# Optimization experiments

Measured on AMD Instinct MI355X. Metric: run time of the kernel, lower is better.

Reference implementation:

```python
import jax, jax.numpy as jnp
import numpy as np

B, T, IN, H, OUT = 64, 256, 512, 1024, 512

def setup_inputs() -> dict:
    key = jax.random.key(0)
    k1, k2, k3, k4 = jax.random.split(key, 4)
    xs = jax.random.normal(k1, (B, T, IN), dtype=jnp.float32)
    # fused gate projections (order: i, f, g, o), scaled like lecun_normal-ish init
    Wi = jax.random.normal(k2, (IN, 4 * H), dtype=jnp.float32) * (1.0 / np.sqrt(IN))
    Wh = jax.random.normal(k3, (H, 4 * H), dtype=jnp.float32) * (1.0 / np.sqrt(H))
    b = jnp.zeros((4 * H,), dtype=jnp.float32)
    Wo = jax.random.normal(k4, (H, OUT), dtype=jnp.float32) * (1.0 / np.sqrt(H))
    bo = jnp.zeros((OUT,), dtype=jnp.float32)
    return {"xs": xs, "Wi": Wi, "Wh": Wh, "b": b, "Wo": Wo, "bo": bo}

def _lstm_scan(xs, Wi, Wh, b):
    # Precompute the input projection for all timesteps at once: [B, T, 4H]
    xp = jnp.einsum('bti,ih->bth', xs, Wi)
    xp = jnp.transpose(xp, (1, 0, 2))  # [T, B, 4H] for scan over time
    h0 = jnp.zeros((xs.shape[0], Wh.shape[0]), dtype=xs.dtype)
    c0 = jnp.zeros_like(h0)
    Hdim = Wh.shape[0]

    def step(carry, xp_t):
        c, h = carry
        gates = xp_t + h @ Wh + b  # [B, 4H]
        i, f, g, o = jnp.split(gates, 4, axis=-1)  # flax order: i, f, g, o
        c_new = jax.nn.sigmoid(f) * c + jax.nn.sigmoid(i) * jnp.tanh(g)
        h_new = jax.nn.sigmoid(o) * jnp.tanh(c_new)
        return (c_new, h_new), h_new

    (_, _), hs = jax.lax.scan(step, (c0, h0), xp)
    return jnp.transpose(hs, (1, 0, 2))  # [B, T, H]

def reference(xs, Wi, Wh, b, Wo, bo):
    zs = _lstm_scan(xs, Wi, Wh, b)          # [B, T, H]
    logits = jnp.einsum('bth,ho->bto', zs, Wo) + bo  # [B, T, OUT]
    return logits
```

## Files before the change

kernel.cpp:

```cpp
#include <hip/hip_runtime.h>
#include <hip/hip_cooperative_groups.h>


#define B_   64
#define T_   256
#define IN_  512
#define H_   1024
#define G4_  4096
#define OUT_ 512
#define KTOT 1536

typedef __bf16 bf8v  __attribute__((ext_vector_type(8)));
typedef float  f4v   __attribute__((ext_vector_type(4)));

__device__ __forceinline__ float sigm(float x) { return 1.f / (1.f + __expf(-x)); }
__device__ __forceinline__ float tanh_f(float x) { return 1.f - 2.f / (__expf(2.f * x) + 1.f); }

__device__ __forceinline__ void store_bf16_wt(__bf16* p, __bf16 v) {
    union { __bf16 b; unsigned short s; } cv; cv.b = v;
    unsigned w = cv.s;
    asm volatile("global_store_short %0, %1, off sc0 sc1"
                 :: "v"(p), "v"(w) : "memory");
}

#define X_PRE(tt, xa0, xa1)                                                   \
    {                                                                         \
        const float* xrow = xs + ((size_t)rowA * T_ + (size_t)(tt)) * IN_ + kq; \
        _Pragma("unroll")                                                     \
        for (int ks = 0; ks < 16; ++ks) {                                     \
            f4v v0 = *(const f4v*)(xrow + ks * 32);                           \
            f4v v1 = *(const f4v*)(xrow + ks * 32 + 4);                       \
            bf8v ah, al;                                                      \
            _Pragma("unroll")                                                 \
            for (int j = 0; j < 4; ++j) {                                     \
                __bf16 h0 = (__bf16)v0[j], h1 = (__bf16)v1[j];                \
                ah[j] = h0;  ah[4 + j] = h1;                                  \
                al[j]     = (__bf16)(v0[j] - (float)h0);                      \
                al[4 + j] = (__bf16)(v1[j] - (float)h1);                      \
            }                                                                 \
            bf8v w = *(const bf8v*)&Wlds[c][ks * 32 + kq];                    \
            xa0 = __builtin_amdgcn_mfma_f32_16x16x32_bf16(ah, w, xa0, 0, 0, 0); \
            xa1 = __builtin_amdgcn_mfma_f32_16x16x32_bf16(al, w, xa1, 0, 0, 0); \
        }                                                                     \
    }

__global__ void __launch_bounds__(256, 1)
lstm_fused(const float* __restrict__ xs, const float* __restrict__ Wi,
           const float* __restrict__ Wh, const float* __restrict__ bias,
           const float* __restrict__ Wo, const float* __restrict__ bo,
           float* __restrict__ out, __bf16* __restrict__ hws,
           unsigned* __restrict__ flags)
{
    __shared__ __bf16 Wlds[16][KTOT + 8];
    __shared__ float  gbuf[64][17];
    __shared__ float  obuf[4][16][17];

    const int tid = threadIdx.x;
    const int blk = blockIdx.x;
    const int j0  = blk * 4;
    const int ob0 = (blk >> 5) * 8;
    const int oc0 = (blk & 31) * 16;

    for (int idx = tid; idx < 16 * KTOT; idx += 256) {
        int k = idx >> 4, c = idx & 15;
        int gc = (c >> 2) * H_ + j0 + (c & 3);
        float w = (k < IN_) ? Wi[(size_t)k * G4_ + gc]
                            : Wh[(size_t)(k - IN_) * G4_ + gc];
        Wlds[c][k] = (__bf16)w;
    }
    __syncthreads();

    const int lane = tid & 63;
    const int wave = tid >> 6;
    const int c    = lane & 15;
    const int quad = lane >> 4;
    const int rowA = wave * 16 + c;
    const int kq   = quad * 8;

    const float biasv = bias[(c >> 2) * H_ + j0 + (c & 3)];

    bf8v wof[8];
    #pragma unroll
    for (int kk = 0; kk < 8; ++kk) {
        int kbase = wave * 256 + kk * 32 + kq;
        #pragma unroll
        for (int j = 0; j < 8; ++j)
            wof[kk][j] = (__bf16)Wo[(size_t)(kbase + j) * OUT_ + oc0 + c];
    }

    float c_reg = 0.f;
    const int bb = tid >> 2;
    const int jo = tid & 3;

    f4v xacc0 = {0.f, 0.f, 0.f, 0.f};
    f4v xacc1 = {0.f, 0.f, 0.f, 0.f};
    X_PRE(0, xacc0, xacc1);

    const size_t bufsz = (size_t)2 * B_ * H_;

    for (int t = 0; t < T_; ++t) {
        const int br = (t + 2) % 3;
        const int bw = t % 3;
        const __bf16* hhi_p = hws + (size_t)br * bufsz;
        const __bf16* hlo_p = hhi_p + B_ * H_;
        __bf16* hhi_c = hws + (size_t)bw * bufsz;
        __bf16* hlo_c = hhi_c + B_ * H_;

        f4v acc0 = xacc0;
        f4v acc1 = xacc1;
        if (t > 0) {
            const __bf16* hh = hhi_p + (size_t)rowA * H_ + kq;
            const __bf16* hl = hlo_p + (size_t)rowA * H_ + kq;
            #pragma unroll
            for (int ks = 0; ks < 32; ++ks) {
                bf8v ah = *(const bf8v*)(hh + ks * 32);
                bf8v al = *(const bf8v*)(hl + ks * 32);
                bf8v w  = *(const bf8v*)&Wlds[c][IN_ + ks * 32 + kq];
                acc0 = __builtin_amdgcn_mfma_f32_16x16x32_bf16(ah, w, acc0, 0, 0, 0);
                acc1 = __builtin_amdgcn_mfma_f32_16x16x32_bf16(al, w, acc1, 0, 0, 0);
            }
        }
        f4v acc = acc0 + acc1;
        #pragma unroll
        for (int r = 0; r < 4; ++r)
            gbuf[wave * 16 + quad * 4 + r][c] = acc[r] + biasv;
        __syncthreads();

        {
            float gi = gbuf[bb][jo];
            float gf = gbuf[bb][4 + jo];
            float gg = gbuf[bb][8 + jo];
            float go = gbuf[bb][12 + jo];
            c_reg = sigm(gf) * c_reg + sigm(gi) * tanh_f(gg);
            float hn = sigm(go) * tanh_f(c_reg);
            __bf16 hh = (__bf16)hn;
            store_bf16_wt(&hhi_c[(size_t)bb * H_ + j0 + jo], hh);
            store_bf16_wt(&hlo_c[(size_t)bb * H_ + j0 + jo], (__bf16)(hn - (float)hh));
        }

        __syncthreads();
        const unsigned tgt = (unsigned)(t + 1);
        if (tid == 0) {
            unsigned* p = &flags[blk * 16];
            asm volatile("global_store_dword %0, %1, off sc0 sc1"
                         :: "v"(p), "v"(tgt) : "memory");
        }

        if (t > 0) {
            f4v oac = {0.f, 0.f, 0.f, 0.f};
            #pragma unroll
            for (int kk = 0; kk < 8; ++kk) {
                int kbase = wave * 256 + kk * 32 + kq;
                bf8v ah = {}, al = {};
                if (c < 8) {
                    ah = *(const bf8v*)&hhi_p[(size_t)(ob0 + c) * H_ + kbase];
                    al = *(const bf8v*)&hlo_p[(size_t)(ob0 + c) * H_ + kbase];
                }
                oac = __builtin_amdgcn_mfma_f32_16x16x32_bf16(ah, wof[kk], oac, 0, 0, 0);
                oac = __builtin_amdgcn_mfma_f32_16x16x32_bf16(al, wof[kk], oac, 0, 0, 0);
            }
            #pragma unroll
            for (int r = 0; r < 4; ++r)
                obuf[wave][quad * 4 + r][c] = oac[r];
        }
        __syncthreads();

        if (t > 0 && tid < 128) {
            int m = tid >> 4, cc = tid & 15;
            float v = obuf[0][m][cc] + obuf[1][m][cc] + obuf[2][m][cc] + obuf[3][m][cc]
                    + bo[oc0 + cc];
            out[(((size_t)(ob0 + m)) * T_ + (t - 1)) * OUT_ + oc0 + cc] = v;
        }

        xacc0 = (f4v){0.f, 0.f, 0.f, 0.f};
        xacc1 = (f4v){0.f, 0.f, 0.f, 0.f};
        if (t + 1 < T_) {
            X_PRE(t + 1, xacc0, xacc1);
        }
        asm volatile("" ::: "memory");

        if (tid < 64) {
            const int lane2 = tid;
            for (;;) {
                unsigned m0 = __hip_atomic_load(&flags[(lane2 * 4 + 0) * 16],
                                                __ATOMIC_RELAXED, __HIP_MEMORY_SCOPE_AGENT);
                unsigned m1 = __hip_atomic_load(&flags[(lane2 * 4 + 1) * 16],
                                                __ATOMIC_RELAXED, __HIP_MEMORY_SCOPE_AGENT);
                unsigned m2 = __hip_atomic_load(&flags[(lane2 * 4 + 2) * 16],
                                                __ATOMIC_RELAXED, __HIP_MEMORY_SCOPE_AGENT);
                unsigned m3 = __hip_atomic_load(&flags[(lane2 * 4 + 3) * 16],
                                                __ATOMIC_RELAXED, __HIP_MEMORY_SCOPE_AGENT);
                bool ok = (m0 >= tgt) & (m1 >= tgt) & (m2 >= tgt) & (m3 >= tgt);
                if (__all(ok)) break;
                __builtin_amdgcn_s_sleep(1);
            }
            __builtin_amdgcn_fence(__ATOMIC_ACQUIRE, "agent");
        }
        __syncthreads();
    }

    {
        const __bf16* hhi_l = hws;
        const __bf16* hlo_l = hws + B_ * H_;
        f4v oac = {0.f, 0.f, 0.f, 0.f};
        #pragma unroll
        for (int kk = 0; kk < 8; ++kk) {
            int kbase = wave * 256 + kk * 32 + kq;
            bf8v ah = {}, al = {};
            if (c < 8) {
                ah = *(const bf8v*)&hhi_l[(size_t)(ob0 + c) * H_ + kbase];
                al = *(const bf8v*)&hlo_l[(size_t)(ob0 + c) * H_ + kbase];
            }
            oac = __builtin_amdgcn_mfma_f32_16x16x32_bf16(ah, wof[kk], oac, 0, 0, 0);
            oac = __builtin_amdgcn_mfma_f32_16x16x32_bf16(al, wof[kk], oac, 0, 0, 0);
        }
        #pragma unroll
        for (int r = 0; r < 4; ++r)
            obuf[wave][quad * 4 + r][c] = oac[r];
        __syncthreads();
        if (tid < 128) {
            int m = tid >> 4, cc = tid & 15;
            float v = obuf[0][m][cc] + obuf[1][m][cc] + obuf[2][m][cc] + obuf[3][m][cc]
                    + bo[oc0 + cc];
            out[(((size_t)(ob0 + m)) * T_ + (T_ - 1)) * OUT_ + oc0 + cc] = v;
        }
    }
}

extern "C" void kernel_launch(void* const* d_in, const int* in_sizes, int n_in,
                              void* d_out, int out_size, void* d_ws, size_t ws_size,
                              hipStream_t stream) {
    const float* xs = (const float*)d_in[0];
    const float* Wi = (const float*)d_in[1];
    const float* Wh = (const float*)d_in[2];
    const float* b  = (const float*)d_in[3];
    const float* Wo = (const float*)d_in[4];
    const float* bo = (const float*)d_in[5];
    float* out = (float*)d_out;

    unsigned* flags = (unsigned*)d_ws;
    __bf16*   hws   = (__bf16*)((char*)d_ws + 65536);

    hipMemsetAsync(d_ws, 0, 32768, stream);

    void* args[] = {(void*)&xs, (void*)&Wi, (void*)&Wh, (void*)&b,
                    (void*)&Wo, (void*)&bo, (void*)&out, (void*)&hws,
                    (void*)&flags};
    hipLaunchCooperativeKernel((void*)lstm_fused, dim3(256), dim3(256), args, 0, stream);
}
```

Before: 4.142 ms.

## Switch LSTM recurrence to single fp16 MFMA with pipelined hidden-state loads

```diff
diff --git a/kernel.cpp b/kernel.cpp
--- a/kernel.cpp
+++ b/kernel.cpp
@@ -10,50 +10,70 @@
 #define OUT_ 512
 #define KTOT 1536
 
-typedef __bf16 bf8v  __attribute__((ext_vector_type(8)));
-typedef float  f4v   __attribute__((ext_vector_type(4)));
+typedef _Float16 f16x8 __attribute__((ext_vector_type(8)));
+typedef float    f4v   __attribute__((ext_vector_type(4)));
 
 __device__ __forceinline__ float sigm(float x) { return 1.f / (1.f + __expf(-x)); }
 __device__ __forceinline__ float tanh_f(float x) { return 1.f - 2.f / (__expf(2.f * x) + 1.f); }
 
-__device__ __forceinline__ void store_bf16_wt(__bf16* p, __bf16 v) {
-    union { __bf16 b; unsigned short s; } cv; cv.b = v;
-    unsigned w = cv.s;
+#define GLOAD(dst, p) \
+    asm volatile("global_load_dwordx4 %0, %1, off sc0 sc1" \
+                 : "=v"(dst) : "v"(p))
+
+#define VM_WAIT(n) do { \
+    asm volatile("s_waitcnt vmcnt(" #n ")"); \
+    __builtin_amdgcn_sched_barrier(0); \
+} while (0)
+
+__device__ __forceinline__ void store_f16_wt(_Float16* p, _Float16 v) {
+    unsigned short s = __builtin_bit_cast(unsigned short, v);
+    unsigned w = s;
     asm volatile("global_store_short %0, %1, off sc0 sc1"
                  :: "v"(p), "v"(w) : "memory");
 }
 
-#define X_PRE(tt, xa0, xa1)                                                   \
+#define X_PRE(tt, xa)                                                         \
     {                                                                         \
         const float* xrow = xs + ((size_t)rowA * T_ + (size_t)(tt)) * IN_ + kq; \
         _Pragma("unroll")                                                     \
         for (int ks = 0; ks < 16; ++ks) {                                     \
             f4v v0 = *(const f4v*)(xrow + ks * 32);                           \
             f4v v1 = *(const f4v*)(xrow + ks * 32 + 4);                       \
-            bf8v ah, al;                                                      \
+            f16x8 a;                                                          \
             _Pragma("unroll")                                                 \
             for (int j = 0; j < 4; ++j) {                                     \
-                __bf16 h0 = (__bf16)v0[j], h1 = (__bf16)v1[j];                \
-                ah[j] = h0;  ah[4 + j] = h1;                                  \
-                al[j]     = (__bf16)(v0[j] - (float)h0);                      \
-                al[4 + j] = (__bf16)(v1[j] - (float)h1);                      \
+                a[j]     = (_Float16)v0[j];                                   \
+                a[4 + j] = (_Float16)v1[j];                                   \
             }                                                                 \
-            bf8v w = *(const bf8v*)&Wlds[c][ks * 32 + kq];                    \
-            xa0 = __builtin_amdgcn_mfma_f32_16x16x32_bf16(ah, w, xa0, 0, 0, 0); \
-            xa1 = __builtin_amdgcn_mfma_f32_16x16x32_bf16(al, w, xa1, 0, 0, 0); \
+            f16x8 w = *(const f16x8*)&Wlds[c][ks * 32 + kq];                  \
+            xa = __builtin_amdgcn_mfma_f32_16x16x32_f16(a, w, xa, 0, 0, 0);   \
         }                                                                     \
+    }
+
+#define GISSUE(Areg, kb)                                                      \
+    _Pragma("unroll")                                                         \
+    for (int i = 0; i < 8; ++i) {                                             \
+        GLOAD(Areg[i], hp + ((kb) + i) * 32);                                 \
+    }
+
+#define GCONSUME(Areg, kb)                                                    \
+    _Pragma("unroll")                                                         \
+    for (int i = 0; i < 8; ++i) {                                             \
+        f16x8 w = *(const f16x8*)&Wlds[c][IN_ + ((kb) + i) * 32 + kq];        \
+        acc = __builtin_amdgcn_mfma_f32_16x16x32_f16(                         \
+            __builtin_bit_cast(f16x8, Areg[i]), w, acc, 0, 0, 0);             \
     }
 
 __global__ void __launch_bounds__(256, 1)
 lstm_fused(const float* __restrict__ xs, const float* __restrict__ Wi,
            const float* __restrict__ Wh, const float* __restrict__ bias,
            const float* __restrict__ Wo, const float* __restrict__ bo,
-           float* __restrict__ out, __bf16* __restrict__ hws,
+           float* __restrict__ out, _Float16* __restrict__ hws,
            unsigned* __restrict__ flags)
 {
-    __shared__ __bf16 Wlds[16][KTOT + 8];
-    __shared__ float  gbuf[64][17];
-    __shared__ float  obuf[4][16][17];
+    __shared__ _Float16 Wlds[16][KTOT + 8];
+    __shared__ float    gbuf[64][17];
+    __shared__ float    obuf[4][16][17];
 
     const int tid = threadIdx.x;
     const int blk = blockIdx.x;
@@ -66,7 +86,7 @@
         int gc = (c >> 2) * H_ + j0 + (c & 3);
         float w = (k < IN_) ? Wi[(size_t)k * G4_ + gc]
                             : Wh[(size_t)(k - IN_) * G4_ + gc];
-        Wlds[c][k] = (__bf16)w;
+        Wlds[c][k] = (_Float16)w;
     }
     __syncthreads();
 
@@ -79,48 +99,48 @@
 
     const float biasv = bias[(c >> 2) * H_ + j0 + (c & 3)];
 
-    bf8v wof[8];
+    f16x8 wof[8];
     #pragma unroll
     for (int kk = 0; kk < 8; ++kk) {
         int kbase = wave * 256 + kk * 32 + kq;
         #pragma unroll
         for (int j = 0; j < 8; ++j)
-            wof[kk][j] = (__bf16)Wo[(size_t)(kbase + j) * OUT_ + oc0 + c];
+            wof[kk][j] = (_Float16)Wo[(size_t)(kbase + j) * OUT_ + oc0 + c];
     }
 
     float c_reg = 0.f;
     const int bb = tid >> 2;
     const int jo = tid & 3;
 
-    f4v xacc0 = {0.f, 0.f, 0.f, 0.f};
-    f4v xacc1 = {0.f, 0.f, 0.f, 0.f};
-    X_PRE(0, xacc0, xacc1);
-
-    const size_t bufsz = (size_t)2 * B_ * H_;
+    f4v xacc = {0.f, 0.f, 0.f, 0.f};
+    X_PRE(0, xacc);
+
+    const size_t bufsz = (size_t)B_ * H_;
 
     for (int t = 0; t < T_; ++t) {
+        asm volatile("" ::: "memory");
         const int br = (t + 2) % 3;
         const int bw = t % 3;
-        const __bf16* hhi_p = hws + (size_t)br * bufsz;
-        const __bf16* hlo_p = hhi_p + B_ * H_;
-        __bf16* hhi_c = hws + (size_t)bw * bufsz;
-        __bf16* hlo_c = hhi_c + B_ * H_;
-
-        f4v acc0 = xacc0;
-        f4v acc1 = xacc1;
+        const _Float16* h_p = hws + (size_t)br * bufsz;
+        _Float16*       h_c = hws + (size_t)bw * bufsz;
+
+        f4v acc = xacc;
         if (t > 0) {
-            const __bf16* hh = hhi_p + (size_t)rowA * H_ + kq;
-            const __bf16* hl = hlo_p + (size_t)rowA * H_ + kq;
-            #pragma unroll
-            for (int ks = 0; ks < 32; ++ks) {
-                bf8v ah = *(const bf8v*)(hh + ks * 32);
-                bf8v al = *(const bf8v*)(hl + ks * 32);
-                bf8v w  = *(const bf8v*)&Wlds[c][IN_ + ks * 32 + kq];
-                acc0 = __builtin_amdgcn_mfma_f32_16x16x32_bf16(ah, w, acc0, 0, 0, 0);
-                acc1 = __builtin_amdgcn_mfma_f32_16x16x32_bf16(al, w, acc1, 0, 0, 0);
-            }
-        }
-        f4v acc = acc0 + acc1;
+            const _Float16* hp = h_p + (size_t)rowA * H_ + kq;
+            f4v A0[8], A1[8];
+            GISSUE(A0, 0);
+            GISSUE(A1, 8);
+            VM_WAIT(8);
+            GCONSUME(A0, 0);
+            GISSUE(A0, 16);
+            VM_WAIT(8);
+            GCONSUME(A1, 8);
+            GISSUE(A1, 24);
+            VM_WAIT(8);
+            GCONSUME(A0, 16);
+            VM_WAIT(0);
+            GCONSUME(A1, 24);
+        }
         #pragma unroll
         for (int r = 0; r < 4; ++r)
             gbuf[wave * 16 + quad * 4 + r][c] = acc[r] + biasv;
@@ -133,9 +153,7 @@
             float go = gbuf[bb][12 + jo];
             c_reg = sigm(gf) * c_reg + sigm(gi) * tanh_f(gg);
             float hn = sigm(go) * tanh_f(c_reg);
-            __bf16 hh = (__bf16)hn;
-            store_bf16_wt(&hhi_c[(size_t)bb * H_ + j0 + jo], hh);
-            store_bf16_wt(&hlo_c[(size_t)bb * H_ + j0 + jo], (__bf16)(hn - (float)hh));
+            store_f16_wt(&h_c[(size_t)bb * H_ + j0 + jo], (_Float16)hn);
         }
 
         __syncthreads();
@@ -147,18 +165,22 @@
         }
 
         if (t > 0) {
+            f4v Oh[8];
+            #pragma unroll
+            for (int kk = 0; kk < 8; ++kk)
+                Oh[kk] = (f4v){0.f, 0.f, 0.f, 0.f};
+            const _Float16* orow = h_p + (size_t)(ob0 + c) * H_;
+            if (c < 8) {
+                #pragma unroll
+                for (int kk = 0; kk < 8; ++kk)
+                    GLOAD(Oh[kk], orow + wave * 256 + kk * 32 + kq);
+            }
+            VM_WAIT(0);
             f4v oac = {0.f, 0.f, 0.f, 0.f};
             #pragma unroll
-            for (int kk = 0; kk < 8; ++kk) {
-                int kbase = wave * 256 + kk * 32 + kq;
-                bf8v ah = {}, al = {};
-                if (c < 8) {
-                    ah = *(const bf8v*)&hhi_p[(size_t)(ob0 + c) * H_ + kbase];
-                    al = *(const bf8v*)&hlo_p[(size_t)(ob0 + c) * H_ + kbase];
-                }
-                oac = __builtin_amdgcn_mfma_f32_16x16x32_bf16(ah, wof[kk], oac, 0, 0, 0);
-                oac = __builtin_amdgcn_mfma_f32_16x16x32_bf16(al, wof[kk], oac, 0, 0, 0);
-            }
+            for (int kk = 0; kk < 8; ++kk)
+                oac = __builtin_amdgcn_mfma_f32_16x16x32_f16(
+                    __builtin_bit_cast(f16x8, Oh[kk]), wof[kk], oac, 0, 0, 0);
             #pragma unroll
             for (int r = 0; r < 4; ++r)
                 obuf[wave][quad * 4 + r][c] = oac[r];
@@ -172,10 +194,9 @@
             out[(((size_t)(ob0 + m)) * T_ + (t - 1)) * OUT_ + oc0 + cc] = v;
         }
 
-        xacc0 = (f4v){0.f, 0.f, 0.f, 0.f};
-        xacc1 = (f4v){0.f, 0.f, 0.f, 0.f};
+        xacc = (f4v){0.f, 0.f, 0.f, 0.f};
         if (t + 1 < T_) {
-            X_PRE(t + 1, xacc0, xacc1);
+            X_PRE(t + 1, xacc);
         }
         asm volatile("" ::: "memory");
 
@@ -194,26 +215,28 @@
                 if (__all(ok)) break;
                 __builtin_amdgcn_s_sleep(1);
             }
-            __builtin_amdgcn_fence(__ATOMIC_ACQUIRE, "agent");
         }
         __syncthreads();
     }
 
     {
-        const __bf16* hhi_l = hws;
-        const __bf16* hlo_l = hws + B_ * H_;
+        const _Float16* h_l = hws;
+        f4v Oh[8];
+        #pragma unroll
+        for (int kk = 0; kk < 8; ++kk)
+            Oh[kk] = (f4v){0.f, 0.f, 0.f, 0.f};
+        const _Float16* orow = h_l + (size_t)(ob0 + c) * H_;
+        if (c < 8) {
+            #pragma unroll
+            for (int kk = 0; kk < 8; ++kk)
+                GLOAD(Oh[kk], orow + wave * 256 + kk * 32 + kq);
+        }
+        VM_WAIT(0);
         f4v oac = {0.f, 0.f, 0.f, 0.f};
         #pragma unroll
-        for (int kk = 0; kk < 8; ++kk) {
-            int kbase = wave * 256 + kk * 32 + kq;
-            bf8v ah = {}, al = {};
-            if (c < 8) {
-                ah = *(const bf8v*)&hhi_l[(size_t)(ob0 + c) * H_ + kbase];
-                al = *(const bf8v*)&hlo_l[(size_t)(ob0 + c) * H_ + kbase];
-            }
-            oac = __builtin_amdgcn_mfma_f32_16x16x32_bf16(ah, wof[kk], oac, 0, 0, 0);
-            oac = __builtin_amdgcn_mfma_f32_16x16x32_bf16(al, wof[kk], oac, 0, 0, 0);
-        }
+        for (int kk = 0; kk < 8; ++kk)
+            oac = __builtin_amdgcn_mfma_f32_16x16x32_f16(
+                __builtin_bit_cast(f16x8, Oh[kk]), wof[kk], oac, 0, 0, 0);
         #pragma unroll
         for (int r = 0; r < 4; ++r)
             obuf[wave][quad * 4 + r][c] = oac[r];
@@ -238,8 +261,8 @@
     const float* bo = (const float*)d_in[5];
     float* out = (float*)d_out;
 
-    unsigned* flags = (unsigned*)d_ws;
-    __bf16*   hws   = (__bf16*)((char*)d_ws + 65536);
+    unsigned*  flags = (unsigned*)d_ws;
+    _Float16*  hws   = (_Float16*)((char*)d_ws + 65536);
 
     hipMemsetAsync(d_ws, 0, 32768, stream);
 
```

Result: faster. 4.014 ms (-3.1%).
